# Optimization experiments

Measured on AMD Instinct MI355X. Metric: run time of the kernel, lower is better.

## Reference

```python
import jax, jax.numpy as jnp
import numpy as np

NUM_HEADS = 16
HEAD_DIM = 64
SCALE = HEAD_DIM ** (-0.5)


def setup_inputs() -> dict:
    key = jax.random.key(0)
    ks = jax.random.split(key, 7)
    B, T, S, D = 8, 1024, 1500, 1024
    std = 1.0 / np.sqrt(D)
    return {
        "x": jax.random.normal(ks[0], (B, T, D), jnp.float32),
        "k": jax.random.normal(ks[1], (B, S, D), jnp.float32),
        "v": jax.random.normal(ks[2], (B, S, D), jnp.float32),
        "wq": jax.random.normal(ks[3], (D, D), jnp.float32) * std,
        "bq": jnp.zeros((D,), jnp.float32),
        "wo": jax.random.normal(ks[4], (D, D), jnp.float32) * std,
        "bo": jnp.zeros((D,), jnp.float32),
    }


def reference(x, k, v, wq, bq, wo, bo):
    B, T, D = x.shape
    H, Dh = NUM_HEADS, HEAD_DIM
    # q_proj (torch Linear: x @ W^T + b), pre-scaled
    q = (jnp.einsum("btd,ed->bte", x, wq) + bq) * SCALE
    q = q.reshape(B, T, H, Dh)                      # bthd
    kh = k.reshape(B, -1, H, Dh)                    # bshd
    vh = v.reshape(B, -1, H, Dh)
    scores = jnp.einsum("bthd,bshd->bhts", q, kh)   # full [B,H,T,S]
    probs = jax.nn.softmax(scores, axis=-1)
    out = jnp.einsum("bhts,bshd->bthd", probs, vh).reshape(B, T, D)
    return jnp.einsum("btd,ed->bte", out, wo) + bo
```

## Files before the change

### kernel.cpp

```cpp
#include <hip/hip_runtime.h>

typedef __attribute__((ext_vector_type(8))) short short8;
typedef __attribute__((ext_vector_type(4))) float floatx4;

#define B_ 8
#define T_ 1024
#define S_ 1500
#define SP 1536
#define D_ 1024
#define H_ 16
#define DH 64
#define SCALE_ 0.125f

__device__ __forceinline__ unsigned short f2bf(float f) {
  unsigned u = __float_as_uint(f);
  u += 0x7fffu + ((u >> 16) & 1u);
  return (unsigned short)(u >> 16);
}

__device__ __forceinline__ floatx4 mfma16(short8 a, short8 b, floatx4 c) {
  return __builtin_amdgcn_mfma_f32_16x16x32_bf16(a, b, c, 0, 0, 0);
}

__global__ void cast_bf16_kernel(const float* __restrict__ src,
                                 unsigned short* __restrict__ dst, int n4) {
  int i = blockIdx.x * blockDim.x + threadIdx.x;
  if (i < n4) {
    float4 v = ((const float4*)src)[i];
    ushort4 o;
    o.x = f2bf(v.x); o.y = f2bf(v.y); o.z = f2bf(v.z); o.w = f2bf(v.w);
    ((ushort4*)dst)[i] = o;
  }
}

__global__ void pack_k_kernel(const float* __restrict__ k,
                              unsigned short* __restrict__ kb) {
  int i = blockIdx.x * blockDim.x + threadIdx.x;
  int dh4 = (i & 15) * 4;
  int j = i >> 4;
  int s = j % SP;
  int bh = j / SP;
  if (bh >= B_ * H_) return;
  int b = bh >> 4, h = bh & 15;
  int p = s & 31;
  int src = (s & ~31) + ((p >> 2) & 3) * 8 + ((p >> 4) & 1) * 4 + (p & 3);
  ushort4 o;
  if (src < S_) {
    float4 v = *(const float4*)(k + (((size_t)(b * S_ + src) * H_ + h) * DH) + dh4);
    o.x = f2bf(v.x); o.y = f2bf(v.y); o.z = f2bf(v.z); o.w = f2bf(v.w);
  } else {
    o = make_ushort4(0, 0, 0, 0);
  }
  *(ushort4*)(kb + ((size_t)bh * SP + s) * DH + dh4) = o;
}

__global__ void pack_vt_kernel(const float* __restrict__ v,
                               unsigned short* __restrict__ vt) {
  __shared__ unsigned short tile[64][72];
  int st = blockIdx.x, bh = blockIdx.y;
  int b = bh >> 4, h = bh & 15;
  int s0 = st * 64;
  int t = threadIdx.x;
  for (int i = t; i < 1024; i += 256) {
    int sl = i >> 4, dh4 = (i & 15) * 4;
    float4 val = make_float4(0.f, 0.f, 0.f, 0.f);
    if (s0 + sl < S_)
      val = *(const float4*)(v + ((size_t)((b * S_ + s0 + sl) * H_ + h)) * DH + dh4);
    tile[dh4 + 0][sl] = f2bf(val.x);
    tile[dh4 + 1][sl] = f2bf(val.y);
    tile[dh4 + 2][sl] = f2bf(val.z);
    tile[dh4 + 3][sl] = f2bf(val.w);
  }
  __syncthreads();
  for (int i = t; i < 1024; i += 256) {
    int d = i >> 4, s4 = (i & 15) * 4;
    ushort4 o;
    o.x = tile[d][s4]; o.y = tile[d][s4 + 1]; o.z = tile[d][s4 + 2]; o.w = tile[d][s4 + 3];
    *(ushort4*)(vt + ((size_t)bh * DH + d) * SP + s0 + s4) = o;
  }
}

#define BK 32
#define ASTR 40
__global__ __launch_bounds__(256) void gemm_bt(const unsigned short* __restrict__ A,
                                               const unsigned short* __restrict__ Bm,
                                               const float* __restrict__ bias,
                                               void* __restrict__ outp, int epi) {
  __shared__ unsigned short As[128 * ASTR];
  __shared__ unsigned short Bs[128 * ASTR];
  const int K = 1024;
  int t = threadIdx.x;
  int m0 = blockIdx.y * 128, n0 = blockIdx.x * 128;
  int w = t >> 6, lane = t & 63, quad = lane >> 4, l16 = lane & 15;
  int mw = (w & 1) * 64, nw = (w >> 1) * 64;
  int lrow = t >> 2, lcol = (t & 3) * 8;

  const unsigned short* Ag = A + (size_t)(m0 + lrow) * K + lcol;
  const unsigned short* Bg = Bm + (size_t)(n0 + lrow) * K + lcol;

  floatx4 acc[4][4];
#pragma unroll
  for (int i = 0; i < 4; i++)
#pragma unroll
    for (int j = 0; j < 4; j++) {
      floatx4 z = {0.f, 0.f, 0.f, 0.f};
      acc[i][j] = z;
    }

  int4 a0 = *(const int4*)(Ag);
  int4 a1 = *(const int4*)(Ag + (size_t)64 * K);
  int4 b0 = *(const int4*)(Bg);
  int4 b1 = *(const int4*)(Bg + (size_t)64 * K);

  for (int kt = 0; kt < K / BK; kt++) {
    __syncthreads();
    *(int4*)&As[lrow * ASTR + lcol] = a0;
    *(int4*)&As[(lrow + 64) * ASTR + lcol] = a1;
    *(int4*)&Bs[lrow * ASTR + lcol] = b0;
    *(int4*)&Bs[(lrow + 64) * ASTR + lcol] = b1;
    __syncthreads();
    if (kt + 1 < K / BK) {
      a0 = *(const int4*)(Ag + (kt + 1) * BK);
      a1 = *(const int4*)(Ag + (size_t)64 * K + (kt + 1) * BK);
      b0 = *(const int4*)(Bg + (kt + 1) * BK);
      b1 = *(const int4*)(Bg + (size_t)64 * K + (kt + 1) * BK);
    }
    short8 af[4], bf[4];
#pragma unroll
    for (int mi = 0; mi < 4; mi++)
      af[mi] = *(const short8*)&As[(mw + mi * 16 + l16) * ASTR + quad * 8];
#pragma unroll
    for (int ni = 0; ni < 4; ni++)
      bf[ni] = *(const short8*)&Bs[(nw + ni * 16 + l16) * ASTR + quad * 8];
#pragma unroll
    for (int mi = 0; mi < 4; mi++)
#pragma unroll
      for (int ni = 0; ni < 4; ni++)
        acc[mi][ni] = mfma16(af[mi], bf[ni], acc[mi][ni]);
  }

#pragma unroll
  for (int mi = 0; mi < 4; mi++)
#pragma unroll
    for (int ni = 0; ni < 4; ni++) {
      int row = m0 + mw + mi * 16 + quad * 4;
      int col = n0 + nw + ni * 16 + l16;
      float bcol = bias[col];
#pragma unroll
      for (int r = 0; r < 4; r++) {
        float val = acc[mi][ni][r] + bcol;
        int rr = row + r;
        if (epi == 0) {
          int b = rr >> 10, tt = rr & 1023, h = col >> 6, dh = col & 63;
          ((unsigned short*)outp)[(((size_t)(b * 16 + h) * 1024) + tt) * 64 + dh] =
              f2bf(val * SCALE_);
        } else {
          ((float*)outp)[(size_t)rr * 1024 + col] = val;
        }
      }
    }
}

__global__ __launch_bounds__(256, 4) void attn_kernel(
    const unsigned short* __restrict__ qs, const unsigned short* __restrict__ kb,
    const unsigned short* __restrict__ vt, unsigned short* __restrict__ ob) {
  __shared__ unsigned short Ks[128 * 72];
  __shared__ unsigned short Vs[64 * 136];
  int ttile = blockIdx.x, bh = blockIdx.y;
  int b = bh >> 4, h = bh & 15;
  int t = threadIdx.x, w = t >> 6, lane = t & 63, quad = lane >> 4, l16 = lane & 15;

  const unsigned short* qp =
      qs + ((size_t)bh * T_ + ttile * 64 + w * 16 + l16) * DH + quad * 8;
  short8 qa0 = *(const short8*)(qp);
  short8 qa1 = *(const short8*)(qp + 32);

  const unsigned short* kbase = kb + (size_t)bh * SP * DH;
  const unsigned short* vbase = vt + (size_t)bh * DH * SP;

  floatx4 o[4];
#pragma unroll
  for (int i = 0; i < 4; i++) {
    floatx4 z = {0.f, 0.f, 0.f, 0.f};
    o[i] = z;
  }
  float mrow = -1e30f, lrow = 0.f;

  for (int s0 = 0; s0 < SP; s0 += 128) {
    __syncthreads();
    {
      const int4* src = (const int4*)(kbase + (size_t)s0 * DH);
      for (int i = t; i < 128 * DH / 8; i += 256) {
        int row = i >> 3, c = i & 7;
        *(int4*)&Ks[row * 72 + c * 8] = src[i];
      }
      for (int i = t; i < 64 * 128 / 8; i += 256) {
        int d = i >> 4, c = i & 15;
        *(int4*)&Vs[d * 136 + c * 8] = *(const int4*)(vbase + (size_t)d * SP + s0 + c * 8);
      }
    }
    __syncthreads();

    floatx4 sc[8];
#pragma unroll
    for (int nb = 0; nb < 8; nb++) {
      short8 k0 = *(const short8*)&Ks[(nb * 16 + l16) * 72 + quad * 8];
      short8 k1 = *(const short8*)&Ks[(nb * 16 + l16) * 72 + 32 + quad * 8];
      floatx4 a = {0.f, 0.f, 0.f, 0.f};
      a = mfma16(k0, qa0, a);
      a = mfma16(k1, qa1, a);
      sc[nb] = a;
    }
    if (s0 + 128 > S_) {
#pragma unroll
      for (int nb = 0; nb < 8; nb++)
#pragma unroll
        for (int r = 0; r < 4; r++) {
          int s_act = s0 + (nb >> 1) * 32 + quad * 8 + (nb & 1) * 4 + r;
          if (s_act >= S_) sc[nb][r] = -1e30f;
        }
    }

    float mx = -1e30f;
#pragma unroll
    for (int nb = 0; nb < 8; nb++) {
      float a0m = fmaxf(sc[nb][0], sc[nb][1]);
      float a1m = fmaxf(sc[nb][2], sc[nb][3]);
      mx = fmaxf(mx, fmaxf(a0m, a1m));
    }
    mx = fmaxf(mx, __shfl_xor(mx, 16));
    mx = fmaxf(mx, __shfl_xor(mx, 32));
    float mnew = fmaxf(mrow, mx);
    float alpha = __expf(mrow - mnew);
    mrow = mnew;
    float rs = 0.f;
#pragma unroll
    for (int nb = 0; nb < 8; nb++) {
#pragma unroll
      for (int r = 0; r < 4; r++) {
        float p = __expf(sc[nb][r] - mnew);
        sc[nb][r] = p;
        rs += p;
      }
    }
    rs += __shfl_xor(rs, 16);
    rs += __shfl_xor(rs, 32);
    lrow = lrow * alpha + rs;
#pragma unroll
    for (int db = 0; db < 4; db++) {
      o[db][0] *= alpha; o[db][1] *= alpha; o[db][2] *= alpha; o[db][3] *= alpha;
    }

#pragma unroll
    for (int c = 0; c < 4; c++) {
      union { short8 v; unsigned short u[8]; } pk;
#pragma unroll
      for (int r = 0; r < 4; r++) {
        pk.u[r] = f2bf(sc[2 * c][r]);
        pk.u[4 + r] = f2bf(sc[2 * c + 1][r]);
      }
#pragma unroll
      for (int db = 0; db < 4; db++) {
        short8 vf = *(const short8*)&Vs[(db * 16 + l16) * 136 + c * 32 + quad * 8];
        o[db] = mfma16(vf, pk.v, o[db]);
      }
    }
  }

  float inv = 1.0f / lrow;
  int tg = ttile * 64 + w * 16 + l16;
#pragma unroll
  for (int db = 0; db < 4; db++) {
    int dh = db * 16 + quad * 4;
    ushort4 st;
    st.x = f2bf(o[db][0] * inv);
    st.y = f2bf(o[db][1] * inv);
    st.z = f2bf(o[db][2] * inv);
    st.w = f2bf(o[db][3] * inv);
    *(ushort4*)(ob + ((size_t)(b * T_ + tg) * H_ + h) * DH + dh) = st;
  }
}

extern "C" void kernel_launch(void* const* d_in, const int* in_sizes, int n_in,
                              void* d_out, int out_size, void* d_ws, size_t ws_size,
                              hipStream_t stream) {
  const float* x  = (const float*)d_in[0];
  const float* k  = (const float*)d_in[1];
  const float* v  = (const float*)d_in[2];
  const float* wq = (const float*)d_in[3];
  const float* bq = (const float*)d_in[4];
  const float* wo = (const float*)d_in[5];
  const float* bo = (const float*)d_in[6];
  float* out = (float*)d_out;

  char* ws = (char*)d_ws;
  unsigned short* xb  = (unsigned short*)(ws + 0);
  unsigned short* wqb = (unsigned short*)(ws + 16777216);
  unsigned short* wob = (unsigned short*)(ws + 18874368);
  unsigned short* kbp = (unsigned short*)(ws + 20971520);
  unsigned short* vtp = (unsigned short*)(ws + 46137344);
  unsigned short* qsp = (unsigned short*)(ws + 71303168);
  unsigned short* obp = (unsigned short*)(ws + 88080384);

  {
    int n4 = B_ * T_ * D_ / 4;
    cast_bf16_kernel<<<n4 / 256, 256, 0, stream>>>(x, xb, n4);
  }
  {
    int n4 = D_ * D_ / 4;
    cast_bf16_kernel<<<n4 / 256, 256, 0, stream>>>(wq, wqb, n4);
    cast_bf16_kernel<<<n4 / 256, 256, 0, stream>>>(wo, wob, n4);
  }
  {
    int groups = B_ * H_ * SP * 16;
    pack_k_kernel<<<groups / 256, 256, 0, stream>>>(k, kbp);
    pack_vt_kernel<<<dim3(SP / 64, B_ * H_), 256, 0, stream>>>(v, vtp);
  }
  gemm_bt<<<dim3(D_ / 128, B_ * T_ / 128), 256, 0, stream>>>(xb, wqb, bq, qsp, 0);
  attn_kernel<<<dim3(T_ / 64, B_ * H_), 256, 0, stream>>>(qsp, kbp, vtp, obp);
  gemm_bt<<<dim3(D_ / 128, B_ * T_ / 128), 256, 0, stream>>>(obp, wob, bo, out, 1);
}
```

Baseline: 358.2 us.

## Enlarge attention tiles, fold log2e into Q scale, fuse cast kernels

The attention kernel now uses 512-thread blocks covering 128 query rows, so each K/V tile staged in shared memory is reused by twice as many queries, with launch bounds raised to match. The Q scale now includes log2(e), which lets the softmax use exp2f in place of __expf. Probability and output packing switch to paired bf16 conversion intrinsics. The three separate fp32-to-bf16 cast launches are merged into one kernel. Larger blocks can reduce occupancy and put more pressure on registers.

After: 470.6 us. 31.4% more time.

```diff
diff --git a/kernel.cpp b/kernel.cpp
--- a/kernel.cpp
+++ b/kernel.cpp
@@ -1,4 +1,5 @@
 #include <hip/hip_runtime.h>
+#include <hip/hip_bf16.h>
 
 typedef __attribute__((ext_vector_type(8))) short short8;
 typedef __attribute__((ext_vector_type(4))) float floatx4;
@@ -10,7 +11,7 @@
 #define D_ 1024
 #define H_ 16
 #define DH 64
-#define SCALE_ 0.125f
+#define SCALE2_ 0.1803368801111244f
 
 __device__ __forceinline__ unsigned short f2bf(float f) {
   unsigned u = __float_as_uint(f);
@@ -22,15 +23,27 @@
   return __builtin_amdgcn_mfma_f32_16x16x32_bf16(a, b, c, 0, 0, 0);
 }
 
-__global__ void cast_bf16_kernel(const float* __restrict__ src,
-                                 unsigned short* __restrict__ dst, int n4) {
+#define N1C (B_ * T_ * D_ / 4)
+#define N2C (D_ * D_ / 4)
+__global__ void cast3_kernel(const float* __restrict__ x, const float* __restrict__ wq,
+                             const float* __restrict__ wo, unsigned short* __restrict__ xb,
+                             unsigned short* __restrict__ wqb,
+                             unsigned short* __restrict__ wob) {
   int i = blockIdx.x * blockDim.x + threadIdx.x;
-  if (i < n4) {
-    float4 v = ((const float4*)src)[i];
-    ushort4 o;
-    o.x = f2bf(v.x); o.y = f2bf(v.y); o.z = f2bf(v.z); o.w = f2bf(v.w);
-    ((ushort4*)dst)[i] = o;
-  }
+  const float* src;
+  unsigned short* dst;
+  int j;
+  if (i < N1C) {
+    src = x; dst = xb; j = i;
+  } else if (i < N1C + N2C) {
+    src = wq; dst = wqb; j = i - N1C;
+  } else {
+    src = wo; dst = wob; j = i - N1C - N2C;
+  }
+  float4 v = ((const float4*)src)[j];
+  ushort4 o;
+  o.x = f2bf(v.x); o.y = f2bf(v.y); o.z = f2bf(v.z); o.w = f2bf(v.w);
+  ((ushort4*)dst)[j] = o;
 }
 
 __global__ void pack_k_kernel(const float* __restrict__ k,
@@ -153,7 +166,7 @@
         if (epi == 0) {
           int b = rr >> 10, tt = rr & 1023, h = col >> 6, dh = col & 63;
           ((unsigned short*)outp)[(((size_t)(b * 16 + h) * 1024) + tt) * 64 + dh] =
-              f2bf(val * SCALE_);
+              f2bf(val * SCALE2_);
         } else {
           ((float*)outp)[(size_t)rr * 1024 + col] = val;
         }
@@ -161,7 +174,7 @@
     }
 }
 
-__global__ __launch_bounds__(256, 4) void attn_kernel(
+__global__ __launch_bounds__(512, 8) void attn_kernel(
     const unsigned short* __restrict__ qs, const unsigned short* __restrict__ kb,
     const unsigned short* __restrict__ vt, unsigned short* __restrict__ ob) {
   __shared__ unsigned short Ks[128 * 72];
@@ -171,7 +184,7 @@
   int t = threadIdx.x, w = t >> 6, lane = t & 63, quad = lane >> 4, l16 = lane & 15;
 
   const unsigned short* qp =
-      qs + ((size_t)bh * T_ + ttile * 64 + w * 16 + l16) * DH + quad * 8;
+      qs + ((size_t)bh * T_ + ttile * 128 + w * 16 + l16) * DH + quad * 8;
   short8 qa0 = *(const short8*)(qp);
   short8 qa1 = *(const short8*)(qp + 32);
 
@@ -190,11 +203,13 @@
     __syncthreads();
     {
       const int4* src = (const int4*)(kbase + (size_t)s0 * DH);
-      for (int i = t; i < 128 * DH / 8; i += 256) {
+#pragma unroll
+      for (int i = t; i < 128 * DH / 8; i += 512) {
         int row = i >> 3, c = i & 7;
         *(int4*)&Ks[row * 72 + c * 8] = src[i];
       }
-      for (int i = t; i < 64 * 128 / 8; i += 256) {
+#pragma unroll
+      for (int i = t; i < 64 * 128 / 8; i += 512) {
         int d = i >> 4, c = i & 15;
         *(int4*)&Vs[d * 136 + c * 8] = *(const int4*)(vbase + (size_t)d * SP + s0 + c * 8);
       }
@@ -231,14 +246,14 @@
     mx = fmaxf(mx, __shfl_xor(mx, 16));
     mx = fmaxf(mx, __shfl_xor(mx, 32));
     float mnew = fmaxf(mrow, mx);
-    float alpha = __expf(mrow - mnew);
+    float alpha = exp2f(mrow - mnew);
     mrow = mnew;
     float rs = 0.f;
 #pragma unroll
     for (int nb = 0; nb < 8; nb++) {
 #pragma unroll
       for (int r = 0; r < 4; r++) {
-        float p = __expf(sc[nb][r] - mnew);
+        float p = exp2f(sc[nb][r] - mnew);
         sc[nb][r] = p;
         rs += p;
       }
@@ -253,12 +268,11 @@
 
 #pragma unroll
     for (int c = 0; c < 4; c++) {
-      union { short8 v; unsigned short u[8]; } pk;
-#pragma unroll
-      for (int r = 0; r < 4; r++) {
-        pk.u[r] = f2bf(sc[2 * c][r]);
-        pk.u[4 + r] = f2bf(sc[2 * c + 1][r]);
-      }
+      union { short8 v; __hip_bfloat162 h[4]; } pk;
+      pk.h[0] = __float22bfloat162_rn(make_float2(sc[2 * c][0], sc[2 * c][1]));
+      pk.h[1] = __float22bfloat162_rn(make_float2(sc[2 * c][2], sc[2 * c][3]));
+      pk.h[2] = __float22bfloat162_rn(make_float2(sc[2 * c + 1][0], sc[2 * c + 1][1]));
+      pk.h[3] = __float22bfloat162_rn(make_float2(sc[2 * c + 1][2], sc[2 * c + 1][3]));
 #pragma unroll
       for (int db = 0; db < 4; db++) {
         short8 vf = *(const short8*)&Vs[(db * 16 + l16) * 136 + c * 32 + quad * 8];
@@ -268,16 +282,14 @@
   }
 
   float inv = 1.0f / lrow;
-  int tg = ttile * 64 + w * 16 + l16;
+  int tg = ttile * 128 + w * 16 + l16;
 #pragma unroll
   for (int db = 0; db < 4; db++) {
     int dh = db * 16 + quad * 4;
-    ushort4 st;
-    st.x = f2bf(o[db][0] * inv);
-    st.y = f2bf(o[db][1] * inv);
-    st.z = f2bf(o[db][2] * inv);
-    st.w = f2bf(o[db][3] * inv);
-    *(ushort4*)(ob + ((size_t)(b * T_ + tg) * H_ + h) * DH + dh) = st;
+    union { ushort4 s4; __hip_bfloat162 h[2]; } st;
+    st.h[0] = __float22bfloat162_rn(make_float2(o[db][0] * inv, o[db][1] * inv));
+    st.h[1] = __float22bfloat162_rn(make_float2(o[db][2] * inv, o[db][3] * inv));
+    *(ushort4*)(ob + ((size_t)(b * T_ + tg) * H_ + h) * DH + dh) = st.s4;
   }
 }
 
@@ -303,13 +315,8 @@
   unsigned short* obp = (unsigned short*)(ws + 88080384);
 
   {
-    int n4 = B_ * T_ * D_ / 4;
-    cast_bf16_kernel<<<n4 / 256, 256, 0, stream>>>(x, xb, n4);
-  }
-  {
-    int n4 = D_ * D_ / 4;
-    cast_bf16_kernel<<<n4 / 256, 256, 0, stream>>>(wq, wqb, n4);
-    cast_bf16_kernel<<<n4 / 256, 256, 0, stream>>>(wo, wob, n4);
+    int blocks = (N1C + 2 * N2C) / 256;
+    cast3_kernel<<<blocks, 256, 0, stream>>>(x, wq, wo, xb, wqb, wob);
   }
   {
     int groups = B_ * H_ * SP * 16;
@@ -317,6 +324,6 @@
     pack_vt_kernel<<<dim3(SP / 64, B_ * H_), 256, 0, stream>>>(v, vtp);
   }
   gemm_bt<<<dim3(D_ / 128, B_ * T_ / 128), 256, 0, stream>>>(xb, wqb, bq, qsp, 0);
-  attn_kernel<<<dim3(T_ / 64, B_ * H_), 256, 0, stream>>>(qsp, kbp, vtp, obp);
+  attn_kernel<<<dim3(T_ / 128, B_ * H_), 512, 0, stream>>>(qsp, kbp, vtp, obp);
   gemm_bt<<<dim3(D_ / 128, B_ * T_ / 128), 256, 0, stream>>>(obp, wob, bo, out, 1);
 }
```
